# Optimization experiments

Measured on AMD Instinct MI355X. Metric: run time of the kernel, lower is better.

The kernel has to match this reference:

```python
import jax, jax.numpy as jnp
import numpy as np

N_NODES = 50000
N_EDGES = 800000
NODE_IN, EDGE_IN, HIDDEN, OUT = 64, 16, 128, 32


def _gcn_conv(x, edge_index, W, b, num_nodes):
    """PyG GCNConv: symmetric-normalized aggregation with self-loops.
       out = D^{-1/2} (A + I) D^{-1/2} (x @ W) + b
    """
    h = x @ W                                   # [N, H]
    loop = jnp.arange(num_nodes, dtype=edge_index.dtype)
    row = jnp.concatenate([edge_index[0], loop])  # src
    col = jnp.concatenate([edge_index[1], loop])  # dst
    deg = jax.ops.segment_sum(jnp.ones(row.shape[0], dtype=h.dtype), col,
                              num_segments=num_nodes)
    dinv = jnp.where(deg > 0, jax.lax.rsqrt(deg), 0.0)
    norm = dinv[row] * dinv[col]                # [E+N]
    msg = h[row] * norm[:, None]                # gather + scale
    out = jax.ops.segment_sum(msg, col, num_segments=num_nodes)  # scatter-add
    return out + b


def setup_inputs() -> dict:
    key = jax.random.key(0)
    ks = jax.random.split(key, 8)
    s1 = 1.0 / np.sqrt(NODE_IN)
    s2 = 1.0 / np.sqrt(HIDDEN)
    s3 = 1.0 / np.sqrt(HIDDEN * 2 + EDGE_IN)
    return {
        "x": jax.random.normal(ks[0], (N_NODES, NODE_IN), dtype=jnp.float32),
        "edge_index": jax.random.randint(ks[1], (2, N_EDGES), 0, N_NODES,
                                         dtype=jnp.int64),
        "edge_attr": jax.random.normal(ks[2], (N_EDGES, EDGE_IN),
                                       dtype=jnp.float32),
        "W1": jax.random.normal(ks[3], (NODE_IN, HIDDEN), dtype=jnp.float32) * s1,
        "b1": jnp.zeros((HIDDEN,), dtype=jnp.float32),
        "W2": jax.random.normal(ks[4], (HIDDEN, HIDDEN), dtype=jnp.float32) * s2,
        "b2": jnp.zeros((HIDDEN,), dtype=jnp.float32),
        "W_edge": jax.random.normal(ks[5], (HIDDEN * 2 + EDGE_IN, OUT),
                                    dtype=jnp.float32) * s3,
        "b_edge": jnp.zeros((OUT,), dtype=jnp.float32),
    }


def reference(x, edge_index, edge_attr, W1, b1, W2, b2, W_edge, b_edge):
    n = x.shape[0]
    h = jax.nn.relu(_gcn_conv(x, edge_index, W1, b1, n))
    h = jax.nn.relu(_gcn_conv(h, edge_index, W2, b2, n))
    src, dst = edge_index[0], edge_index[1]
    edge_features = jnp.concatenate([h[src], h[dst], edge_attr], axis=1)
    return edge_features @ W_edge + b_edge
```

## Files before the change

### kernel.cpp

```cpp
#include <hip/hip_runtime.h>

#define NN 50000
#define NE 800000

typedef __attribute__((ext_vector_type(8))) short short8v;
typedef __attribute__((ext_vector_type(4))) float f32x4;

__device__ __forceinline__ float bf_lo(unsigned u) { return __uint_as_float(u << 16); }
__device__ __forceinline__ float bf_hi(unsigned u) { return __uint_as_float(u & 0xffff0000u); }
__device__ __forceinline__ unsigned pack_bf2(float a, float b) {
  unsigned ua = __float_as_uint(a);
  ua = (ua + 0x7fffu + ((ua >> 16) & 1u)) >> 16;
  unsigned ub = __float_as_uint(b);
  ub = (ub + 0x7fffu + ((ub >> 16) & 1u)) & 0xffff0000u;
  return ua | ub;
}
__device__ __forceinline__ unsigned short bf16r(float f) {
  unsigned u = __float_as_uint(f);
  u = (u + 0x7fffu + ((u >> 16) & 1u)) >> 16;
  return (unsigned short)u;
}

__global__ void k_prep0(const float* __restrict__ W1, const float* __restrict__ W2,
                        const float* __restrict__ We,
                        unsigned short* __restrict__ W1t,
                        unsigned short* __restrict__ W2t,
                        unsigned short* __restrict__ Wabt,
                        int* cnt) {
  int i = blockIdx.x * 256 + threadIdx.x;
  if (i < NN) cnt[i] = 0;
  if (i < 8192)  { int c = i >> 6, k = i & 63;  W1t[i] = bf16r(W1[k * 128 + c]); }
  if (i < 16384) { int c = i >> 7, k = i & 127; W2t[i] = bf16r(W2[k * 128 + c]); }
  if (i < 8192) {
    int c = i >> 7, k = i & 127;
    float v = (c < 32) ? We[k * 32 + c] : We[(128 + k) * 32 + (c - 32)];
    Wabt[i] = bf16r(v);
  }
}

__global__ void k_count(const int* __restrict__ dst, int* __restrict__ cnt,
                        int* __restrict__ rank, int e) {
  int i = blockIdx.x * blockDim.x + threadIdx.x;
  if (i < e) rank[i] = atomicAdd(&cnt[dst[i]], 1);
}

__global__ void k_scan1(const int* cnt, int* offs, int* bsum, int n) {
  __shared__ int s[256];
  int i = blockIdx.x * 256 + threadIdx.x;
  int v = (i < n) ? cnt[i] : 0;
  s[threadIdx.x] = v;
  __syncthreads();
  #pragma unroll
  for (int d = 1; d < 256; d <<= 1) {
    int t = (threadIdx.x >= d) ? s[threadIdx.x - d] : 0;
    __syncthreads();
    s[threadIdx.x] += t;
    __syncthreads();
  }
  if (i < n) offs[i] = s[threadIdx.x] - v;
  if (threadIdx.x == 255) bsum[blockIdx.x] = s[255];
}

__global__ void k_scan2(int* bsum, int* offsN, int nb) {
  __shared__ int s[256];
  int v = (threadIdx.x < nb) ? bsum[threadIdx.x] : 0;
  s[threadIdx.x] = v;
  __syncthreads();
  #pragma unroll
  for (int d = 1; d < 256; d <<= 1) {
    int t = (threadIdx.x >= d) ? s[threadIdx.x - d] : 0;
    __syncthreads();
    s[threadIdx.x] += t;
    __syncthreads();
  }
  if (threadIdx.x < nb) bsum[threadIdx.x] = s[threadIdx.x] - v;
  if (threadIdx.x == 255) *offsN = s[255];
}

__global__ void k_scan3p(int* __restrict__ offs, const int* __restrict__ bsum,
                         const int* __restrict__ cnt, float* __restrict__ dinv,
                         const float* __restrict__ x, unsigned* __restrict__ xs) {
  int i = blockIdx.x * blockDim.x + threadIdx.x;
  if (i >= NN * 32) return;
  int v = i >> 5, l = i & 31;
  float d = rsqrtf((float)(cnt[v] + 1));
  if (l == 0) {
    offs[v] += bsum[v >> 8];
    dinv[v] = d;
  }
  float2 xv = ((const float2*)(x + (size_t)v * 64))[l];
  xs[(size_t)v * 32 + l] = pack_bf2(xv.x * d, xv.y * d);
}

__global__ void k_fill(const int* __restrict__ src, const int* __restrict__ dst,
                       const int* __restrict__ offs, const int* __restrict__ rank,
                       int* __restrict__ adj, int e) {
  int i = blockIdx.x * blockDim.x + threadIdx.x;
  if (i < e) adj[offs[dst[i]] + rank[i]] = src[i];
}

__global__ __launch_bounds__(256) void k_aggemm1(
    const unsigned* __restrict__ xs, const int* __restrict__ offs,
    const int* __restrict__ adj, const float* __restrict__ dinv,
    const unsigned short* __restrict__ Bt,
    const float* __restrict__ bias,
    unsigned short* __restrict__ outb,
    int n) {
  __shared__ unsigned zd[32][36];
  int lane = threadIdx.x & 63;
  int wid = threadIdx.x >> 6;
  int r0 = blockIdx.x * 32;
  int h = lane >> 5, hl = lane & 31;
  for (int it = 0; it < 4; it++) {
    int loc = wid * 8 + it * 2 + h;
    int node = r0 + loc;
    if (node >= n) node = n - 1;
    float ax[8], ay[8];
    {
      unsigned u = xs[(size_t)node * 32 + hl];
      ax[0] = bf_lo(u); ay[0] = bf_hi(u);
    }
    #pragma unroll
    for (int u = 1; u < 8; u++) { ax[u] = 0.f; ay[u] = 0.f; }
    int s = offs[node], e = offs[node + 1];
    int i = s;
    for (; i + 8 <= e; i += 8) {
      int idx[8];
      #pragma unroll
      for (int u = 0; u < 8; u++) idx[u] = adj[i + u];
      #pragma unroll
      for (int u = 0; u < 8; u++) {
        unsigned uv = xs[(size_t)idx[u] * 32 + hl];
        ax[u] += bf_lo(uv); ay[u] += bf_hi(uv);
      }
    }
    for (; i < e; i++) {
      unsigned uv = xs[(size_t)adj[i] * 32 + hl];
      ax[0] += bf_lo(uv); ay[0] += bf_hi(uv);
    }
    float sx = ((ax[0] + ax[1]) + (ax[2] + ax[3])) + ((ax[4] + ax[5]) + (ax[6] + ax[7]));
    float sy = ((ay[0] + ay[1]) + (ay[2] + ay[3])) + ((ay[4] + ay[5]) + (ay[6] + ay[7]));
    float d = dinv[node];
    zd[loc][hl] = pack_bf2(sx * d, sy * d);
  }
  __syncthreads();
  int wr = wid >> 1, wc = wid & 1;
  int lr = lane & 15;
  int lk = (lane >> 4) * 8;
  f32x4 acc[4];
  #pragma unroll
  for (int ct = 0; ct < 4; ct++) acc[ct] = (f32x4){0.f, 0.f, 0.f, 0.f};
  #pragma unroll
  for (int ks = 0; ks < 64; ks += 32) {
    short8v a = *reinterpret_cast<const short8v*>(
        (const unsigned short*)&zd[wr * 16 + lr][0] + lk + ks);
    #pragma unroll
    for (int ct = 0; ct < 4; ct++) {
      const unsigned short* bp = Bt + (size_t)(wc * 64 + ct * 16 + lr) * 64 + lk + ks;
      short8v b = *reinterpret_cast<const short8v*>(bp);
      acc[ct] = __builtin_amdgcn_mfma_f32_16x16x32_bf16(a, b, acc[ct], 0, 0, 0);
    }
  }
  int rbase = r0 + wr * 16 + (lane >> 4) * 4;
  #pragma unroll
  for (int ct = 0; ct < 4; ct++) {
    int col = wc * 64 + ct * 16 + lr;
    float bv = bias[col];
    #pragma unroll
    for (int rg = 0; rg < 4; rg++) {
      int row = rbase + rg;
      if (row >= n) continue;
      float v = fmaxf(acc[ct][rg] + bv, 0.f);
      outb[(size_t)row * 128 + col] = bf16r(v * dinv[row]);
    }
  }
}

__global__ __launch_bounds__(256) void k_aggemm2(
    const unsigned* __restrict__ hw,
    const int* __restrict__ offs, const int* __restrict__ adj,
    const float* __restrict__ dinv,
    const unsigned short* __restrict__ Bt,
    const unsigned short* __restrict__ Wabt,
    const float* __restrict__ bias,
    unsigned short* __restrict__ PQb,
    int n) {
  __shared__ unsigned ztd[32][68];
  __shared__ unsigned short hs2[32][136];
  int lane = threadIdx.x & 63;
  int wid = threadIdx.x >> 6;
  int r0 = blockIdx.x * 32;
  for (int it = 0; it < 8; it++) {
    int loc = wid * 8 + it;
    int node = r0 + loc;
    if (node >= n) node = n - 1;
    float ax[8], ay[8];
    {
      unsigned u = hw[(size_t)node * 64 + lane];
      ax[0] = bf_lo(u); ay[0] = bf_hi(u);
    }
    #pragma unroll
    for (int u = 1; u < 8; u++) { ax[u] = 0.f; ay[u] = 0.f; }
    int s = offs[node], e = offs[node + 1];
    int i = s;
    for (; i + 8 <= e; i += 8) {
      int idx[8];
      #pragma unroll
      for (int u = 0; u < 8; u++) idx[u] = adj[i + u];
      #pragma unroll
      for (int u = 0; u < 8; u++) {
        unsigned uv = hw[(size_t)idx[u] * 64 + lane];
        ax[u] += bf_lo(uv); ay[u] += bf_hi(uv);
      }
    }
    for (; i < e; i++) {
      unsigned uv = hw[(size_t)adj[i] * 64 + lane];
      ax[0] += bf_lo(uv); ay[0] += bf_hi(uv);
    }
    float sx = ((ax[0] + ax[1]) + (ax[2] + ax[3])) + ((ax[4] + ax[5]) + (ax[6] + ax[7]));
    float sy = ((ay[0] + ay[1]) + (ay[2] + ay[3])) + ((ay[4] + ay[5]) + (ay[6] + ay[7]));
    float d = dinv[node];
    ztd[loc][lane] = pack_bf2(sx * d, sy * d);
  }
  __syncthreads();
  int wr = wid >> 1, wc = wid & 1;
  int lr = lane & 15;
  int lk = (lane >> 4) * 8;
  f32x4 acc[4];
  #pragma unroll
  for (int ct = 0; ct < 4; ct++) acc[ct] = (f32x4){0.f, 0.f, 0.f, 0.f};
  #pragma unroll
  for (int ks = 0; ks < 128; ks += 32) {
    short8v a = *reinterpret_cast<const short8v*>(
        (const unsigned short*)&ztd[wr * 16 + lr][0] + lk + ks);
    #pragma unroll
    for (int ct = 0; ct < 4; ct++) {
      const unsigned short* bp = Bt + (size_t)(wc * 64 + ct * 16 + lr) * 128 + lk + ks;
      short8v b = *reinterpret_cast<const short8v*>(bp);
      acc[ct] = __builtin_amdgcn_mfma_f32_16x16x32_bf16(a, b, acc[ct], 0, 0, 0);
    }
  }
  int rloc = wr * 16 + (lane >> 4) * 4;
  #pragma unroll
  for (int ct = 0; ct < 4; ct++) {
    int col = wc * 64 + ct * 16 + lr;
    float bv = bias[col];
    #pragma unroll
    for (int rg = 0; rg < 4; rg++)
      hs2[rloc + rg][col] = bf16r(fmaxf(acc[ct][rg] + bv, 0.f));
  }
  __syncthreads();
  f32x4 acc2[2];
  acc2[0] = (f32x4){0.f, 0.f, 0.f, 0.f};
  acc2[1] = (f32x4){0.f, 0.f, 0.f, 0.f};
  #pragma unroll
  for (int ks = 0; ks < 128; ks += 32) {
    short8v a2 = *reinterpret_cast<const short8v*>(&hs2[wr * 16 + lr][lk + ks]);
    #pragma unroll
    for (int ct = 0; ct < 2; ct++) {
      const unsigned short* wp = Wabt + (size_t)(wc * 32 + ct * 16 + lr) * 128 + lk + ks;
      short8v b = *reinterpret_cast<const short8v*>(wp);
      acc2[ct] = __builtin_amdgcn_mfma_f32_16x16x32_bf16(a2, b, acc2[ct], 0, 0, 0);
    }
  }
  #pragma unroll
  for (int ct = 0; ct < 2; ct++) {
    int col = wc * 32 + ct * 16 + lr;
    #pragma unroll
    for (int rg = 0; rg < 4; rg++) {
      int row = r0 + wr * 16 + (lane >> 4) * 4 + rg;
      if (row < n) PQb[(size_t)row * 64 + col] = bf16r(acc2[ct][rg]);
    }
  }
}

__global__ __launch_bounds__(256) void k_edge5(const int* __restrict__ src,
                                               const int* __restrict__ dst,
                                               const float* __restrict__ ea,
                                               const unsigned* __restrict__ PQw,
                                               const float* __restrict__ We,
                                               const float* __restrict__ be,
                                               float* __restrict__ out, int ne) {
  __shared__ int sidx[64];
  __shared__ int didx[64];
  __shared__ float eas[64][16];
  __shared__ float wcs[16][32];
  __shared__ float bes[32];
  int tid = threadIdx.x;
  int ebase = blockIdx.x * 64;
  if (tid < 128)
    ((float4*)wcs)[tid] = ((const float4*)(We + 256 * 32))[tid];
  if (tid < 32) bes[tid] = be[tid];
  if (tid >= 128 && tid < 192) sidx[tid - 128] = src[ebase + tid - 128];
  if (tid >= 192)              didx[tid - 192] = dst[ebase + tid - 192];
  {
    int row = tid >> 2, q = tid & 3;
    ((float4*)eas[row])[q] = ((const float4*)(ea + (size_t)(ebase + row) * 16))[q];
  }
  __syncthreads();
  int l = tid & 15;
  int grp = tid >> 4;
  unsigned pw[4], qw[4];
  int el[4];
  #pragma unroll
  for (int u = 0; u < 4; u++) el[u] = u * 16 + grp;
  #pragma unroll
  for (int u = 0; u < 4; u++) {
    int s = sidx[el[u]];
    int d = didx[el[u]];
    pw[u] = PQw[(size_t)s * 32 + l];
    qw[u] = PQw[(size_t)d * 32 + 16 + l];
  }
  int c0 = 2 * l;
  #pragma unroll
  for (int u = 0; u < 4; u++) {
    int e = ebase + el[u];
    float a0 = bf_lo(pw[u]) + bf_lo(qw[u]) + bes[c0];
    float a1 = bf_hi(pw[u]) + bf_hi(qw[u]) + bes[c0 + 1];
    #pragma unroll
    for (int k = 0; k < 16; k++) {
      float ev = eas[el[u]][k];
      a0 += ev * wcs[k][c0];
      a1 += ev * wcs[k][c0 + 1];
    }
    ((float2*)(out + (size_t)e * 32))[l] = make_float2(a0, a1);
  }
}

extern "C" void kernel_launch(void* const* d_in, const int* in_sizes, int n_in,
                              void* d_out, int out_size, void* d_ws, size_t ws_size,
                              hipStream_t stream) {
  const float* x  = (const float*)d_in[0];
  const int*   ei = (const int*)d_in[1];
  const float* ea = (const float*)d_in[2];
  const float* W1 = (const float*)d_in[3];
  const float* b1 = (const float*)d_in[4];
  const float* W2 = (const float*)d_in[5];
  const float* b2 = (const float*)d_in[6];
  const float* We = (const float*)d_in[7];
  const float* be = (const float*)d_in[8];
  float* out = (float*)d_out;
  const int* src = ei;
  const int* dst = ei + NE;

  char* w = (char*)d_ws;
  auto alloc = [&](size_t b) {
    void* p = (void*)w;
    w += (b + 255) & ~(size_t)255;
    return p;
  };
  int* cnt    = (int*)alloc(NN * 4);
  int* offs   = (int*)alloc((NN + 1) * 4);
  int* bsum   = (int*)alloc(256 * 4);
  int* adj    = (int*)alloc((size_t)NE * 4);
  int* rank   = (int*)alloc((size_t)NE * 4);
  float* dinv = (float*)alloc(NN * 4);
  unsigned* xs  = (unsigned*)alloc((size_t)NN * 32 * 4);
  unsigned* h1s = (unsigned*)alloc((size_t)NN * 64 * 4);
  unsigned short* pqb  = (unsigned short*)alloc((size_t)NN * 64 * 2);
  unsigned short* w1t  = (unsigned short*)alloc(8192 * 2);
  unsigned short* w2t  = (unsigned short*)alloc(16384 * 2);
  unsigned short* wabt = (unsigned short*)alloc(8192 * 2);

  const int nblkN = (NN + 255) / 256;
  const int nblkE = (NE + 255) / 256;

  k_prep0<<<nblkN, 256, 0, stream>>>(W1, W2, We, w1t, w2t, wabt, cnt);
  k_count<<<nblkE, 256, 0, stream>>>(dst, cnt, rank, NE);
  k_scan1<<<nblkN, 256, 0, stream>>>(cnt, offs, bsum, NN);
  k_scan2<<<1, 256, 0, stream>>>(bsum, offs + NN, nblkN);
  k_scan3p<<<(NN * 32 + 255) / 256, 256, 0, stream>>>(offs, bsum, cnt, dinv, x, xs);
  k_fill<<<nblkE, 256, 0, stream>>>(src, dst, offs, rank, adj, NE);

  const int mgBlk = (NN + 31) / 32;
  k_aggemm1<<<mgBlk, 256, 0, stream>>>(xs, offs, adj, dinv, w1t, b1,
                                       (unsigned short*)h1s, NN);
  k_aggemm2<<<mgBlk, 256, 0, stream>>>(h1s, offs, adj, dinv, w2t, wabt, b2,
                                       pqb, NN);
  k_edge5<<<NE / 64, 256, 0, stream>>>(src, dst, ea, (const unsigned*)pqb,
                                       We, be, out, NE);
}
```

Before: 239.9 us.

## Split layer-2 aggregation from GEMM and widen edge kernel to 128 edges

The fused layer-2 aggregate+GEMM kernel is split into a separate gather kernel, one wavefront per node with a 16-wide unrolled gather, and a standalone two-stage MFMA GEMM that reads the aggregated rows from global memory. The aim is to remove the load imbalance of one wave serially handling 8 nodes, and to expose more memory-level parallelism in the gather. The edge output kernel now processes 128 edges per block with 8 gathers in flight per thread. The split adds a full round trip of the aggregated features through global memory and one extra launch, and reuses the h1 buffer for the PQ output.

```diff
diff --git a/kernel.cpp b/kernel.cpp
--- a/kernel.cpp
+++ b/kernel.cpp
@@ -176,63 +176,77 @@
   }
 }
 
-__global__ __launch_bounds__(256) void k_aggemm2(
-    const unsigned* __restrict__ hw,
-    const int* __restrict__ offs, const int* __restrict__ adj,
-    const float* __restrict__ dinv,
+__global__ void k_agg128(const unsigned* __restrict__ hs,
+                         const int* __restrict__ offs, const int* __restrict__ adj,
+                         const float* __restrict__ dinv, unsigned* __restrict__ z,
+                         int n) {
+  int node = blockIdx.x * 4 + (threadIdx.x >> 6);
+  if (node >= n) return;
+  int lane = threadIdx.x & 63;
+  float ax[8], ay[8];
+  {
+    unsigned u = hs[(size_t)node * 64 + lane];
+    ax[0] = bf_lo(u); ay[0] = bf_hi(u);
+  }
+  #pragma unroll
+  for (int u = 1; u < 8; u++) { ax[u] = 0.f; ay[u] = 0.f; }
+  int s = offs[node], e = offs[node + 1];
+  int i = s;
+  for (; i + 16 <= e; i += 16) {
+    int idx[16];
+    #pragma unroll
+    for (int u = 0; u < 16; u++) idx[u] = adj[i + u];
+    unsigned uv[16];
+    #pragma unroll
+    for (int u = 0; u < 16; u++) uv[u] = hs[(size_t)idx[u] * 64 + lane];
+    #pragma unroll
+    for (int u = 0; u < 16; u++) {
+      ax[u & 7] += bf_lo(uv[u]); ay[u & 7] += bf_hi(uv[u]);
+    }
+  }
+  for (; i + 8 <= e; i += 8) {
+    int idx[8];
+    #pragma unroll
+    for (int u = 0; u < 8; u++) idx[u] = adj[i + u];
+    #pragma unroll
+    for (int u = 0; u < 8; u++) {
+      unsigned uv = hs[(size_t)idx[u] * 64 + lane];
+      ax[u] += bf_lo(uv); ay[u] += bf_hi(uv);
+    }
+  }
+  for (; i < e; i++) {
+    unsigned uv = hs[(size_t)adj[i] * 64 + lane];
+    ax[0] += bf_lo(uv); ay[0] += bf_hi(uv);
+  }
+  float sx = ((ax[0] + ax[1]) + (ax[2] + ax[3])) + ((ax[4] + ax[5]) + (ax[6] + ax[7]));
+  float sy = ((ay[0] + ay[1]) + (ay[2] + ay[3])) + ((ay[4] + ay[5]) + (ay[6] + ay[7]));
+  float d = dinv[node];
+  z[(size_t)node * 64 + lane] = pack_bf2(sx * d, sy * d);
+}
+
+__global__ __launch_bounds__(256) void k_mgemm2pq(
+    const unsigned short* __restrict__ A,
     const unsigned short* __restrict__ Bt,
     const unsigned short* __restrict__ Wabt,
     const float* __restrict__ bias,
     unsigned short* __restrict__ PQb,
     int n) {
-  __shared__ unsigned ztd[32][68];
-  __shared__ unsigned short hs2[32][136];
+  __shared__ unsigned short hs[32][136];
   int lane = threadIdx.x & 63;
   int wid = threadIdx.x >> 6;
+  int wr = wid >> 1, wc = wid & 1;
   int r0 = blockIdx.x * 32;
-  for (int it = 0; it < 8; it++) {
-    int loc = wid * 8 + it;
-    int node = r0 + loc;
-    if (node >= n) node = n - 1;
-    float ax[8], ay[8];
-    {
-      unsigned u = hw[(size_t)node * 64 + lane];
-      ax[0] = bf_lo(u); ay[0] = bf_hi(u);
-    }
-    #pragma unroll
-    for (int u = 1; u < 8; u++) { ax[u] = 0.f; ay[u] = 0.f; }
-    int s = offs[node], e = offs[node + 1];
-    int i = s;
-    for (; i + 8 <= e; i += 8) {
-      int idx[8];
-      #pragma unroll
-      for (int u = 0; u < 8; u++) idx[u] = adj[i + u];
-      #pragma unroll
-      for (int u = 0; u < 8; u++) {
-        unsigned uv = hw[(size_t)idx[u] * 64 + lane];
-        ax[u] += bf_lo(uv); ay[u] += bf_hi(uv);
-      }
-    }
-    for (; i < e; i++) {
-      unsigned uv = hw[(size_t)adj[i] * 64 + lane];
-      ax[0] += bf_lo(uv); ay[0] += bf_hi(uv);
-    }
-    float sx = ((ax[0] + ax[1]) + (ax[2] + ax[3])) + ((ax[4] + ax[5]) + (ax[6] + ax[7]));
-    float sy = ((ay[0] + ay[1]) + (ay[2] + ay[3])) + ((ay[4] + ay[5]) + (ay[6] + ay[7]));
-    float d = dinv[node];
-    ztd[loc][lane] = pack_bf2(sx * d, sy * d);
-  }
-  __syncthreads();
-  int wr = wid >> 1, wc = wid & 1;
   int lr = lane & 15;
   int lk = (lane >> 4) * 8;
+  int arow = r0 + wr * 16 + lr;
+  if (arow >= n) arow = n - 1;
+  const unsigned short* arp = A + (size_t)arow * 128 + lk;
   f32x4 acc[4];
   #pragma unroll
   for (int ct = 0; ct < 4; ct++) acc[ct] = (f32x4){0.f, 0.f, 0.f, 0.f};
   #pragma unroll
   for (int ks = 0; ks < 128; ks += 32) {
-    short8v a = *reinterpret_cast<const short8v*>(
-        (const unsigned short*)&ztd[wr * 16 + lr][0] + lk + ks);
+    short8v a = *reinterpret_cast<const short8v*>(arp + ks);
     #pragma unroll
     for (int ct = 0; ct < 4; ct++) {
       const unsigned short* bp = Bt + (size_t)(wc * 64 + ct * 16 + lr) * 128 + lk + ks;
@@ -247,7 +261,7 @@
     float bv = bias[col];
     #pragma unroll
     for (int rg = 0; rg < 4; rg++)
-      hs2[rloc + rg][col] = bf16r(fmaxf(acc[ct][rg] + bv, 0.f));
+      hs[rloc + rg][col] = bf16r(fmaxf(acc[ct][rg] + bv, 0.f));
   }
   __syncthreads();
   f32x4 acc2[2];
@@ -255,7 +269,7 @@
   acc2[1] = (f32x4){0.f, 0.f, 0.f, 0.f};
   #pragma unroll
   for (int ks = 0; ks < 128; ks += 32) {
-    short8v a2 = *reinterpret_cast<const short8v*>(&hs2[wr * 16 + lr][lk + ks]);
+    short8v a2 = *reinterpret_cast<const short8v*>(&hs[wr * 16 + lr][lk + ks]);
     #pragma unroll
     for (int ct = 0; ct < 2; ct++) {
       const unsigned short* wp = Wabt + (size_t)(wc * 32 + ct * 16 + lr) * 128 + lk + ks;
@@ -274,52 +288,55 @@
   }
 }
 
-__global__ __launch_bounds__(256) void k_edge5(const int* __restrict__ src,
+__global__ __launch_bounds__(256) void k_edge6(const int* __restrict__ src,
                                                const int* __restrict__ dst,
                                                const float* __restrict__ ea,
                                                const unsigned* __restrict__ PQw,
                                                const float* __restrict__ We,
                                                const float* __restrict__ be,
                                                float* __restrict__ out, int ne) {
-  __shared__ int sidx[64];
-  __shared__ int didx[64];
-  __shared__ float eas[64][16];
+  __shared__ int sidx[128];
+  __shared__ int didx[128];
+  __shared__ float eas[128][16];
   __shared__ float wcs[16][32];
   __shared__ float bes[32];
   int tid = threadIdx.x;
-  int ebase = blockIdx.x * 64;
-  if (tid < 128)
+  int ebase = blockIdx.x * 128;
+  if (tid < 128) {
     ((float4*)wcs)[tid] = ((const float4*)(We + 256 * 32))[tid];
+    sidx[tid] = src[ebase + tid];
+  } else {
+    didx[tid - 128] = dst[ebase + tid - 128];
+  }
   if (tid < 32) bes[tid] = be[tid];
-  if (tid >= 128 && tid < 192) sidx[tid - 128] = src[ebase + tid - 128];
-  if (tid >= 192)              didx[tid - 192] = dst[ebase + tid - 192];
-  {
-    int row = tid >> 2, q = tid & 3;
+  #pragma unroll
+  for (int j = 0; j < 2; j++) {
+    int q4 = tid * 2 + j;
+    int row = q4 >> 2, q = q4 & 3;
     ((float4*)eas[row])[q] = ((const float4*)(ea + (size_t)(ebase + row) * 16))[q];
   }
   __syncthreads();
   int l = tid & 15;
   int grp = tid >> 4;
-  unsigned pw[4], qw[4];
-  int el[4];
-  #pragma unroll
-  for (int u = 0; u < 4; u++) el[u] = u * 16 + grp;
-  #pragma unroll
-  for (int u = 0; u < 4; u++) {
-    int s = sidx[el[u]];
-    int d = didx[el[u]];
+  unsigned pw[8], qw[8];
+  #pragma unroll
+  for (int u = 0; u < 8; u++) {
+    int el = u * 16 + grp;
+    int s = sidx[el];
+    int d = didx[el];
     pw[u] = PQw[(size_t)s * 32 + l];
     qw[u] = PQw[(size_t)d * 32 + 16 + l];
   }
   int c0 = 2 * l;
   #pragma unroll
-  for (int u = 0; u < 4; u++) {
-    int e = ebase + el[u];
+  for (int u = 0; u < 8; u++) {
+    int el = u * 16 + grp;
+    int e = ebase + el;
     float a0 = bf_lo(pw[u]) + bf_lo(qw[u]) + bes[c0];
     float a1 = bf_hi(pw[u]) + bf_hi(qw[u]) + bes[c0 + 1];
     #pragma unroll
     for (int k = 0; k < 16; k++) {
-      float ev = eas[el[u]][k];
+      float ev = eas[el][k];
       a0 += ev * wcs[k][c0];
       a1 += ev * wcs[k][c0 + 1];
     }
@@ -357,10 +374,11 @@
   float* dinv = (float*)alloc(NN * 4);
   unsigned* xs  = (unsigned*)alloc((size_t)NN * 32 * 4);
   unsigned* h1s = (unsigned*)alloc((size_t)NN * 64 * 4);
-  unsigned short* pqb  = (unsigned short*)alloc((size_t)NN * 64 * 2);
+  unsigned* z12 = (unsigned*)alloc((size_t)NN * 64 * 4);
   unsigned short* w1t  = (unsigned short*)alloc(8192 * 2);
   unsigned short* w2t  = (unsigned short*)alloc(16384 * 2);
   unsigned short* wabt = (unsigned short*)alloc(8192 * 2);
+  unsigned short* pqb = (unsigned short*)h1s;
 
   const int nblkN = (NN + 255) / 256;
   const int nblkE = (NE + 255) / 256;
@@ -375,8 +393,9 @@
   const int mgBlk = (NN + 31) / 32;
   k_aggemm1<<<mgBlk, 256, 0, stream>>>(xs, offs, adj, dinv, w1t, b1,
                                        (unsigned short*)h1s, NN);
-  k_aggemm2<<<mgBlk, 256, 0, stream>>>(h1s, offs, adj, dinv, w2t, wabt, b2,
-                                       pqb, NN);
-  k_edge5<<<NE / 64, 256, 0, stream>>>(src, dst, ea, (const unsigned*)pqb,
-                                       We, be, out, NE);
-}
+  k_agg128<<<(NN + 3) / 4, 256, 0, stream>>>(h1s, offs, adj, dinv, z12, NN);
+  k_mgemm2pq<<<mgBlk, 256, 0, stream>>>((const unsigned short*)z12, w2t, wabt,
+                                        b2, pqb, NN);
+  k_edge6<<<NE / 128, 256, 0, stream>>>(src, dst, ea, (const unsigned*)pqb,
+                                        We, be, out, NE);
+}
```

Result: faster. 231.8 us (-3.4%).
